# Kernel optimization log

Hardware: AMD Instinct MI355X
Metric: run time of the kernel (lower is better)

Reference implementation:

```python
import jax, jax.numpy as jnp
import numpy as np

N_NODES = 50000

def setup_inputs() -> dict:
    key = jax.random.key(0)
    k1, k2, k3, k4, k5 = jax.random.split(key, 5)
    x = jax.random.normal(k1, (50000, 512), dtype=jnp.float32)
    edge_row = jax.random.randint(k2, (800000,), 0, N_NODES, dtype=jnp.int64)
    edge_col = jax.random.randint(k3, (800000,), 0, N_NODES, dtype=jnp.int64)
    edge_val = jax.random.uniform(k4, (800000,), dtype=jnp.float32)
    # init like torch: uniform(-stdv, stdv), stdv = 1/sqrt(out_features)
    stdv = 1.0 / np.sqrt(96.0)
    weight = jax.random.uniform(k5, (512, 96), minval=-stdv, maxval=stdv, dtype=jnp.float32)
    return {"x": x, "edge_row": edge_row, "edge_col": edge_col, "edge_val": edge_val, "weight": weight}

def reference(x, edge_row, edge_col, edge_val, weight):
    # support = X @ W  -- dense GEMM [N, F_in] x [F_in, F_out]
    support = x @ weight
    # sparse adjacency matmul: out[row] += val * support[col]
    msgs = edge_val[:, None] * support[edge_col]          # [E, F_out]
    out = jax.ops.segment_sum(msgs, edge_row, num_segments=N_NODES)
    # act = ReLU (module default); bias=False
    return jax.nn.relu(out)
```

## Files before the change

### kernel.cpp

```cpp
#include <hip/hip_runtime.h>

#define N_NODES 50000
#define F_IN    512
#define F_OUT   96
#define N_EDGES 800000

#define RPB    128
#define NBKT   391
#define CAP    2560
#define ECHUNK 4096
#define NCHUNK ((N_EDGES + ECHUNK - 1) / ECHUNK)
#define GEMM_BLOCKS ((N_NODES + 63) / 64)

typedef __attribute__((ext_vector_type(8))) short bf16x8;
typedef __attribute__((ext_vector_type(4))) float f32x4;

__device__ __forceinline__ unsigned short f2bf(float f) {
    unsigned int u = __float_as_uint(f);
    unsigned int r = (u + 0x7FFFu + ((u >> 16) & 1u)) >> 16;
    return (unsigned short)r;
}
__device__ __forceinline__ float bf2f(unsigned short h) {
    return __uint_as_float(((unsigned int)h) << 16);
}

__global__ __launch_bounds__(256) void k_wcast(const float* __restrict__ w,
                                               unsigned short* __restrict__ wTq,
                                               int* __restrict__ bcnt) {
    if (blockIdx.x == 0) {
        const int t = threadIdx.x;
        bcnt[t] = 0;
        if (t < 144) bcnt[256 + t] = 0;
    }
    const int i = blockIdx.x * 256 + threadIdx.x;
    if (i < F_OUT * F_IN) {
        const int j    = i & 7;
        const int lane = (i >> 3) & 63;
        const int ks   = (i >> 9) & 1;
        const int tp   = i >> 10;
        const int t    = tp % 6;
        const int p    = tp / 6;
        const int lr   = lane & 15;
        const int kg   = lane >> 4;
        const int n    = t * 16 + lr;
        const int k    = p * 64 + ks * 32 + kg * 8 + j;
        wTq[i] = f2bf(w[(size_t)k * F_OUT + n]);
    }
}

__global__ __launch_bounds__(256) void k_fused(const float* __restrict__ x,
                                               const unsigned short* __restrict__ wTq,
                                               unsigned short* __restrict__ support,
                                               const int* __restrict__ erow,
                                               const int* __restrict__ ecol,
                                               const float* __restrict__ eval,
                                               int* __restrict__ bcnt,
                                               float2* __restrict__ bucket) {
    __shared__ __align__(16) char smem[16384];
    const int tid = threadIdx.x;

    if (blockIdx.x < NCHUNK) {
        int* hist  = (int*)smem;
        int* gbase = hist + 400;
        int* lcur  = gbase + 400;
        for (int i = tid; i < NBKT; i += 256) { hist[i] = 0; lcur[i] = 0; }
        __syncthreads();

        const int base = blockIdx.x * ECHUNK;
        const int n = min(ECHUNK, N_EDGES - base);

        for (int i = tid; i < n; i += 256)
            atomicAdd(&hist[erow[base + i] >> 7], 1);
        __syncthreads();

        for (int b = tid; b < NBKT; b += 256)
            gbase[b] = hist[b] ? atomicAdd(&bcnt[b], hist[b]) : 0;
        __syncthreads();

        for (int i = tid; i < n; i += 256) {
            const int r = erow[base + i];
            const int b = r >> 7;
            const int pos = gbase[b] + atomicAdd(&lcur[b], 1);
            if (pos >= 0 && pos < CAP)
                bucket[(size_t)b * CAP + pos] = make_float2(
                    __int_as_float(((r & 127) << 16) | ecol[base + i]),
                    eval[base + i]);
        }
        return;
    }

    unsigned short (*sX)[64 * 64] = (unsigned short (*)[64 * 64])smem;

    const int lane = tid & 63;
    const int wave = tid >> 6;
    const int r0   = (blockIdx.x - NCHUNK) * 64;
    const int lr   = lane & 15;
    const int kg   = lane >> 4;

    f32x4 acc[6];
    #pragma unroll
    for (int t = 0; t < 6; ++t) acc[t] = (f32x4){0.f, 0.f, 0.f, 0.f};

    float4 xr[4];

    auto XLOAD = [&](int p) {
        #pragma unroll
        for (int i = 0; i < 4; ++i) {
            const int chunk = i * 256 + tid;
            const int row   = chunk >> 4;
            const int c     = chunk & 15;
            int gr = r0 + row;
            if (gr > N_NODES - 1) gr = N_NODES - 1;
            xr[i] = *reinterpret_cast<const float4*>(x + (size_t)gr * F_IN + p * 64 + c * 4);
        }
    };
    auto XWRITE = [&](int buf) {
        char* xb = (char*)&sX[buf][0];
        #pragma unroll
        for (int i = 0; i < 4; ++i) {
            const int chunk = i * 256 + tid;
            const int row   = chunk >> 4;
            const int c     = chunk & 15;
            ushort4 h;
            h.x = f2bf(xr[i].x); h.y = f2bf(xr[i].y);
            h.z = f2bf(xr[i].z); h.w = f2bf(xr[i].w);
            const int byte = (c * 8) ^ ((row & 7) << 4);
            *reinterpret_cast<ushort4*>(xb + row * 128 + byte) = h;
        }
    };
    auto COMPUTE = [&](int buf, int p) {
        const char* xb = (const char*)&sX[buf][0];
        const int xrow = wave * 16 + lr;
        const unsigned short* bbase = wTq + ((size_t)p * 12) * 512 + lane * 8;
        #pragma unroll
        for (int ks = 0; ks < 2; ++ks) {
            const int off = (ks * 64 + kg * 16) ^ ((xrow & 7) << 4);
            const bf16x8 af = *reinterpret_cast<const bf16x8*>(xb + xrow * 128 + off);
            #pragma unroll
            for (int t = 0; t < 6; ++t) {
                const bf16x8 bq = *reinterpret_cast<const bf16x8*>(
                    bbase + (t * 2 + ks) * 512);
                acc[t] = __builtin_amdgcn_mfma_f32_16x16x32_bf16(af, bq, acc[t], 0, 0, 0);
            }
        }
    };

    XLOAD(0);
    XWRITE(0);
    __syncthreads();
    for (int p = 0; p < 8; ++p) {
        if (p < 7) XLOAD(p + 1);
        COMPUTE(p & 1, p);
        if (p < 7) XWRITE((p + 1) & 1);
        __syncthreads();
    }

    #pragma unroll
    for (int t = 0; t < 6; ++t) {
        #pragma unroll
        for (int r = 0; r < 4; ++r) {
            const int row = r0 + wave * 16 + kg * 4 + r;
            if (row < N_NODES)
                support[(size_t)row * F_OUT + t * 16 + lr] = f2bf(acc[t][r]);
        }
    }
}

__global__ __launch_bounds__(256) void kS_sort(const int* __restrict__ bcnt,
                                               const float2* __restrict__ bucket,
                                               float2* __restrict__ bucket2,
                                               int* __restrict__ rowOffs) {
    __shared__ int cnt[RPB];
    __shared__ int sc[RPB];
    __shared__ int rbase[RPB];
    __shared__ int rcur[RPB];
    const int b   = blockIdx.x;
    const int tid = threadIdx.x;

    if (tid < RPB) { cnt[tid] = 0; rcur[tid] = 0; }
    __syncthreads();

    const int beg = b * CAP;
    const int n   = min(bcnt[b], CAP);

    for (int i = tid; i < n; i += 256)
        atomicAdd(&cnt[(__float_as_int(bucket[beg + i].x) >> 16) & 127], 1);
    __syncthreads();

    if (tid < RPB) sc[tid] = cnt[tid];
    __syncthreads();
    #pragma unroll
    for (int off = 1; off < RPB; off <<= 1) {
        int a = 0;
        if (tid < RPB && tid >= off) a = sc[tid - off];
        __syncthreads();
        if (tid < RPB) sc[tid] += a;
        __syncthreads();
    }
    if (tid < RPB) {
        const int rb = beg + sc[tid] - cnt[tid];
        rbase[tid] = rb;
        rowOffs[b * 129 + tid] = rb;
    }
    if (tid == RPB) rowOffs[b * 129 + RPB] = beg + n;
    __syncthreads();

    for (int i = tid; i < n; i += 256) {
        const float2 ev  = bucket[beg + i];
        const int    key = __float_as_int(ev.x);
        const int    r   = (key >> 16) & 127;
        const int    pos = rbase[r] + atomicAdd(&rcur[r], 1);
        bucket2[pos] = make_float2(__int_as_float(key & 0xFFFF), ev.y);
    }
}

__global__ __launch_bounds__(256) void k_gather(const int* __restrict__ rowOffs,
                                                const float2* __restrict__ bucket2,
                                                const unsigned short* __restrict__ support,
                                                float* __restrict__ out) {
    const int gid = blockIdx.x * 256 + threadIdx.x;
    if (gid >= N_NODES * 6) return;
    const int r   = gid / 6;
    const int f16 = gid - r * 6;

    const int idx = (r >> 7) * 129 + (r & 127);
    const int beg = rowOffs[idx];
    const int end = rowOffs[idx + 1];

    float acc[16];
    #pragma unroll
    for (int j = 0; j < 16; ++j) acc[j] = 0.f;

    for (int i = beg; i < end; ++i) {
        const float2 cv = bucket2[i];
        const int   c = __float_as_int(cv.x);
        const float v = cv.y;
        const unsigned short* sp = support + (size_t)c * F_OUT + f16 * 16;
        const bf16x8 s0 = *reinterpret_cast<const bf16x8*>(sp);
        const bf16x8 s1 = *reinterpret_cast<const bf16x8*>(sp + 8);
        #pragma unroll
        for (int j = 0; j < 8; ++j) {
            acc[j]     = fmaf(v, bf2f((unsigned short)s0[j]), acc[j]);
            acc[8 + j] = fmaf(v, bf2f((unsigned short)s1[j]), acc[8 + j]);
        }
    }

    float* o = out + (size_t)r * F_OUT + f16 * 16;
    #pragma unroll
    for (int q = 0; q < 4; ++q) {
        float4 ov;
        ov.x = fmaxf(acc[q * 4 + 0], 0.f);
        ov.y = fmaxf(acc[q * 4 + 1], 0.f);
        ov.z = fmaxf(acc[q * 4 + 2], 0.f);
        ov.w = fmaxf(acc[q * 4 + 3], 0.f);
        *reinterpret_cast<float4*>(o + q * 4) = ov;
    }
}

extern "C" void kernel_launch(void* const* d_in, const int* in_sizes, int n_in,
                              void* d_out, int out_size, void* d_ws, size_t ws_size,
                              hipStream_t stream) {
    const float* x    = (const float*)d_in[0];
    const int*   erow = (const int*)d_in[1];
    const int*   ecol = (const int*)d_in[2];
    const float* eval = (const float*)d_in[3];
    const float* w    = (const float*)d_in[4];
    float*       out  = (float*)d_out;

    unsigned short* support = (unsigned short*)d_ws;
    int*    bcnt    = (int*)((char*)d_ws + 9600000);
    int*    rowOffs = bcnt + 400;
    unsigned short* wTq = (unsigned short*)(rowOffs + 50560);
    float2* bucket  = (float2*)((char*)wTq + 98304);
    float2* bucket2 = bucket + (size_t)NBKT * CAP;

    k_wcast<<<(F_OUT * F_IN + 255) / 256, 256, 0, stream>>>(w, wTq, bcnt);

    k_fused<<<NCHUNK + GEMM_BLOCKS, 256, 0, stream>>>(x, wTq, support,
                                                      erow, ecol, eval,
                                                      bcnt, bucket);

    kS_sort<<<NBKT, 256, 0, stream>>>(bcnt, bucket, bucket2, rowOffs);

    const int gthreads = N_NODES * 6;
    k_gather<<<(gthreads + 255) / 256, 256, 0, stream>>>(rowOffs, bucket2, support, out);
}
```

Measured before the change: 82.21 us.

## Stage X tiles via direct global-to-LDS loads with triple buffering

Replaces the register-staged X load, bf16 conversion and LDS write with global_load_lds 16-byte direct copies into a three-deep fp32 LDS ring, waited on with explicit vmcnt counts and barriers. The bf16 conversion moves to the read side inside COMPUTE, and the XOR swizzle is applied on the global source address. The aim is to cut register pressure and the VALU/LDS-store work in the producer path and to overlap two panels of loads with compute. In exchange LDS use triples to 48KB and LDS reads double in size, which may reduce occupancy and puts conversion ALU work next to the MFMAs.

```diff
diff --git a/kernel.cpp b/kernel.cpp
--- a/kernel.cpp
+++ b/kernel.cpp
@@ -14,6 +14,18 @@
 
 typedef __attribute__((ext_vector_type(8))) short bf16x8;
 typedef __attribute__((ext_vector_type(4))) float f32x4;
+
+typedef const __attribute__((address_space(1))) void* gas_ptr;
+typedef __attribute__((address_space(3))) void* las_ptr;
+
+__device__ __forceinline__ void gload_lds16(const void* g, void* l) {
+    __builtin_amdgcn_global_load_lds((gas_ptr)g, (las_ptr)l, 16, 0, 0);
+}
+
+#define VMCNT_SB(n) do { \
+    asm volatile("s_waitcnt vmcnt(" #n ")" ::: "memory"); \
+    __builtin_amdgcn_sched_barrier(0); \
+} while (0)
 
 __device__ __forceinline__ unsigned short f2bf(float f) {
     unsigned int u = __float_as_uint(f);
@@ -56,7 +68,7 @@
                                                const float* __restrict__ eval,
                                                int* __restrict__ bcnt,
                                                float2* __restrict__ bucket) {
-    __shared__ __align__(16) char smem[16384];
+    __shared__ __align__(16) char smem[49152];
     const int tid = threadIdx.x;
 
     if (blockIdx.x < NCHUNK) {
@@ -89,8 +101,6 @@
         return;
     }
 
-    unsigned short (*sX)[64 * 64] = (unsigned short (*)[64 * 64])smem;
-
     const int lane = tid & 63;
     const int wave = tid >> 6;
     const int r0   = (blockIdx.x - NCHUNK) * 64;
@@ -101,41 +111,36 @@
     #pragma unroll
     for (int t = 0; t < 6; ++t) acc[t] = (f32x4){0.f, 0.f, 0.f, 0.f};
 
-    float4 xr[4];
-
-    auto XLOAD = [&](int p) {
+    auto STAGE = [&](int s, int p) {
+        float* dst = (float*)(smem + s * 16384);
         #pragma unroll
         for (int i = 0; i < 4; ++i) {
             const int chunk = i * 256 + tid;
             const int row   = chunk >> 4;
-            const int c     = chunk & 15;
+            const int s16   = chunk & 15;
             int gr = r0 + row;
             if (gr > N_NODES - 1) gr = N_NODES - 1;
-            xr[i] = *reinterpret_cast<const float4*>(x + (size_t)gr * F_IN + p * 64 + c * 4);
+            const int srcb = (s16 * 16) ^ ((row & 15) << 4);
+            gload_lds16(x + (size_t)gr * F_IN + p * 64 + (srcb >> 2),
+                        dst + chunk * 4);
         }
     };
-    auto XWRITE = [&](int buf) {
-        char* xb = (char*)&sX[buf][0];
-        #pragma unroll
-        for (int i = 0; i < 4; ++i) {
-            const int chunk = i * 256 + tid;
-            const int row   = chunk >> 4;
-            const int c     = chunk & 15;
-            ushort4 h;
-            h.x = f2bf(xr[i].x); h.y = f2bf(xr[i].y);
-            h.z = f2bf(xr[i].z); h.w = f2bf(xr[i].w);
-            const int byte = (c * 8) ^ ((row & 7) << 4);
-            *reinterpret_cast<ushort4*>(xb + row * 128 + byte) = h;
-        }
-    };
-    auto COMPUTE = [&](int buf, int p) {
-        const char* xb = (const char*)&sX[buf][0];
+    auto COMPUTE = [&](int s, int p) {
+        const float* xb = (const float*)(smem + s * 16384);
         const int xrow = wave * 16 + lr;
-        const unsigned short* bbase = wTq + ((size_t)p * 12) * 512 + lane * 8;
+        const unsigned short* bbase = wTq + (size_t)p * 12 * 512 + lane * 8;
         #pragma unroll
         for (int ks = 0; ks < 2; ++ks) {
-            const int off = (ks * 64 + kg * 16) ^ ((xrow & 7) << 4);
-            const bf16x8 af = *reinterpret_cast<const bf16x8*>(xb + xrow * 128 + off);
+            const int byte0 = ks * 128 + kg * 32;
+            const int b0 = byte0        ^ (lr << 4);
+            const int b1 = (byte0 + 16) ^ (lr << 4);
+            const float4 a0 = *reinterpret_cast<const float4*>(xb + xrow * 64 + (b0 >> 2));
+            const float4 a1 = *reinterpret_cast<const float4*>(xb + xrow * 64 + (b1 >> 2));
+            bf16x8 af;
+            af[0] = (short)f2bf(a0.x); af[1] = (short)f2bf(a0.y);
+            af[2] = (short)f2bf(a0.z); af[3] = (short)f2bf(a0.w);
+            af[4] = (short)f2bf(a1.x); af[5] = (short)f2bf(a1.y);
+            af[6] = (short)f2bf(a1.z); af[7] = (short)f2bf(a1.w);
             #pragma unroll
             for (int t = 0; t < 6; ++t) {
                 const bf16x8 bq = *reinterpret_cast<const bf16x8*>(
@@ -145,15 +150,27 @@
         }
     };
 
-    XLOAD(0);
-    XWRITE(0);
-    __syncthreads();
-    for (int p = 0; p < 8; ++p) {
-        if (p < 7) XLOAD(p + 1);
-        COMPUTE(p & 1, p);
-        if (p < 7) XWRITE((p + 1) & 1);
-        __syncthreads();
-    }
+    STAGE(0, 0);
+    STAGE(1, 1);
+
+#define PANEL(p, vm) \
+    do { \
+        if ((p) + 2 < 8) STAGE(((p) + 2) % 3, (p) + 2); \
+        VMCNT_SB(vm); \
+        __builtin_amdgcn_s_barrier(); \
+        COMPUTE((p) % 3, (p)); \
+        __builtin_amdgcn_s_barrier(); \
+    } while (0)
+
+    PANEL(0, 8);
+    PANEL(1, 8);
+    PANEL(2, 8);
+    PANEL(3, 8);
+    PANEL(4, 8);
+    PANEL(5, 8);
+    PANEL(6, 4);
+    PANEL(7, 0);
+#undef PANEL
 
     #pragma unroll
     for (int t = 0; t < 6; ++t) {
```

New measurement: 83.12 us. No clear change (+1.1%).
